# Performance work log

Measured on AMD Instinct MI355X. Metric: run time of the kernel, lower is better.

Reference implementation:

```python
import jax, jax.numpy as jnp
import numpy as np

B, T, D, NH = 4, 2048, 1024, 16
DH = D // NH


def setup_inputs() -> dict:
    key = jax.random.key(0)
    k1, k2, k3 = jax.random.split(key, 3)
    x = jax.random.normal(k1, (B, T, D), dtype=jnp.float32)
    # torch nn.Linear default init scale ~ 1/sqrt(fan_in); keep values sane
    w_qkv = jax.random.normal(k2, (D, 3 * D), dtype=jnp.float32) / np.sqrt(D)
    w_out = jax.random.normal(k3, (D, D), dtype=jnp.float32) / np.sqrt(D)
    return {"x": x, "w_qkv": w_qkv, "w_out": w_out}


def reference(x, w_qkv, w_out):
    Bb, Tt, Dd = x.shape
    # fused QKV projection (Linear, no bias)
    qkv = x @ w_qkv                                  # (B, T, 3D)
    q, k, v = jnp.split(qkv, 3, axis=-1)
    # split heads -> (B, NH, T, DH)
    q = q.reshape(Bb, Tt, NH, DH).transpose(0, 2, 1, 3)
    k = k.reshape(Bb, Tt, NH, DH).transpose(0, 2, 1, 3)
    v = v.reshape(Bb, Tt, NH, DH).transpose(0, 2, 1, 3)
    scale = 1.0 / np.sqrt(DH).astype(np.float32)
    att = jnp.einsum('bhqd,bhkd->bhqk', q, k) * scale  # (B, NH, T, T)
    att = jax.nn.softmax(att, axis=-1)
    y = jnp.einsum('bhqk,bhkd->bhqd', att, v)          # (B, NH, T, DH)
    y = y.transpose(0, 2, 1, 3).reshape(Bb, Tt, Dd)    # merge heads
    return y @ w_out                                   # output projection
```

## Files before the change

kernel.cpp:

```cpp
#include <hip/hip_runtime.h>

#define B  4
#define T  2048
#define D  1024
#define NH 16
#define DH 64
#define MROWS (B*T)

typedef __attribute__((ext_vector_type(8))) short bf16x8;
typedef __attribute__((ext_vector_type(4))) float f32x4;
typedef __attribute__((ext_vector_type(4))) unsigned short u16x4;
typedef __attribute__((address_space(1))) const void gvoid;
typedef __attribute__((address_space(3))) void lvoid;

#define C_EXP 0.18033688011112042f
#define VSWZ(dh) (((((dh) ^ ((dh) >> 2)) & 7)) << 4)

__device__ inline unsigned short f2bf(float f) {
    union { float f; unsigned int u; } v; v.f = f;
    unsigned int r = v.u + 0x7fff + ((v.u >> 16) & 1);
    return (unsigned short)(r >> 16);
}
__device__ inline float bf2f(unsigned short u) {
    union { unsigned int u; float f; } v; v.u = ((unsigned int)u) << 16;
    return v.f;
}
__device__ inline float exp2_fast(float x) {
    float r;
    asm("v_exp_f32 %0, %1" : "=v"(r) : "v"(x));
    return r;
}

__global__ __launch_bounds__(256)
void cast_bf16(const float* __restrict__ in, unsigned short* __restrict__ hi, int n4) {
    for (int i = blockIdx.x * 256 + threadIdx.x; i < n4; i += gridDim.x * 256) {
        const float4 v = ((const float4*)in)[i];
        ushort4 h;
        h.x = f2bf(v.x); h.y = f2bf(v.y); h.z = f2bf(v.z); h.w = f2bf(v.w);
        ((ushort4*)hi)[i] = h;
    }
}

__global__ __launch_bounds__(256)
void split_frag2(const float* __restrict__ Wq, const float* __restrict__ Wo,
                 unsigned short* __restrict__ fq, unsigned short* __restrict__ fo) {
    const int l   = threadIdx.x & 63;
    const int kt  = blockIdx.y;
    const int NKT = D / 32;
    const bool isQ = (blockIdx.x < 3 * D / 64);
    const int bx  = isQ ? blockIdx.x : blockIdx.x - 3 * D / 64;
    const int nt  = bx * 4 + (threadIdx.x >> 6);
    const int N   = isQ ? 3 * D : D;
    const float* Wm = isQ ? Wq : Wo;
    unsigned short* fh = isQ ? fq : fo;
    const int n   = nt * 16 + (l & 15);
    const int k0  = kt * 32 + (l >> 4) * 8;
    const float sc = (isQ && n < D) ? C_EXP : 1.0f;
    bf16x8 hv;
    #pragma unroll
    for (int j = 0; j < 8; ++j)
        hv[j] = (short)f2bf(Wm[(size_t)(k0 + j) * N + n] * sc);
    const size_t o = ((size_t)nt * NKT + kt) * 512 + (size_t)l * 8;
    *(bf16x8*)&fh[o] = hv;
}

template<bool OUT_BF16, bool TWO_PASS>
__global__ __launch_bounds__(256, 3)
void gemm_bdir(const unsigned short* __restrict__ Ahi, const unsigned short* __restrict__ Alo,
               const unsigned short* __restrict__ Bfh,
               void* __restrict__ Cout, int M, int N, int K) {
    __shared__ unsigned char As[2][128 * 128];
    const int tid  = threadIdx.x;
    const int w    = tid >> 6;
    const int lane = tid & 63;
    const int lq   = lane & 15;
    const int lk   = lane >> 4;
    const int wm   = w >> 1;
    const int wn   = w & 1;
    const int NKT  = K / 32;

    const int gx  = gridDim.x;
    const int cpx = gx >> 3;
    const int lin = blockIdx.y * gx + blockIdx.x;
    const int cx  = lin & 7;
    const int j   = lin >> 3;
    const int bn  = (cx * cpx + j % cpx) * 128;
    const int bm  = (j / cpx) * 128;

    const int srow   = lane >> 3;
    const int sidx   = (lane & 7) ^ srow;
    const int shalf  = sidx >> 2;
    const int schunk = sidx & 3;
    const unsigned short* aPtr = TWO_PASS
        ? ((shalf ? Alo : Ahi) + (size_t)(bm + w * 32 + srow) * K + schunk * 8)
        : (Ahi + (size_t)(bm + w * 32 + srow) * K + sidx * 8);

    const unsigned short* bhBase = Bfh + ((size_t)(bn / 16 + wn * 4) * NKT) * 512 + (size_t)lane * 8;

    f32x4 acc[4][4];
    #pragma unroll
    for (int m = 0; m < 4; ++m)
        #pragma unroll
        for (int n = 0; n < 4; ++n) acc[m][n] = f32x4{0.f, 0.f, 0.f, 0.f};

    #pragma unroll
    for (int i = 0; i < 4; ++i)
        __builtin_amdgcn_global_load_lds((gvoid*)(aPtr + (size_t)i * 8 * K),
                                         (lvoid*)&As[0][(w * 32 + i * 8) * 128], 16, 0, 0);
    __syncthreads();

    int cur = 0;
    if constexpr (TWO_PASS) {
        for (int kt = 0; kt < NKT; ++kt) {
            if (kt + 1 < NKT) {
                #pragma unroll
                for (int i = 0; i < 4; ++i)
                    __builtin_amdgcn_global_load_lds(
                        (gvoid*)(aPtr + (size_t)i * 8 * K + (kt + 1) * 32),
                        (lvoid*)&As[cur ^ 1][(w * 32 + i * 8) * 128], 16, 0, 0);
            }
            bf16x8 bh[4];
            #pragma unroll
            for (int n = 0; n < 4; ++n)
                bh[n] = *(const bf16x8*)&bhBase[((size_t)n * NKT + kt) * 512];
            bf16x8 ah[4], al[4];
            #pragma unroll
            for (int m = 0; m < 4; ++m) {
                const int row = wm * 64 + m * 16 + lq;
                const int sw  = row & 7;
                ah[m] = *(const bf16x8*)&As[cur][row * 128 + ((lk ^ sw) << 4)];
                al[m] = *(const bf16x8*)&As[cur][row * 128 + (((4 + lk) ^ sw) << 4)];
            }
            __builtin_amdgcn_s_setprio(1);
            #pragma unroll
            for (int n = 0; n < 4; ++n)
                #pragma unroll
                for (int m = 0; m < 4; ++m) {
                    acc[m][n] = __builtin_amdgcn_mfma_f32_16x16x32_bf16(ah[m], bh[n], acc[m][n], 0, 0, 0);
                    acc[m][n] = __builtin_amdgcn_mfma_f32_16x16x32_bf16(al[m], bh[n], acc[m][n], 0, 0, 0);
                }
            __builtin_amdgcn_s_setprio(0);
            __syncthreads();
            cur ^= 1;
        }
    } else {
        const int NS = K / 64;
        for (int s2 = 0; s2 < NS; ++s2) {
            if (s2 + 1 < NS) {
                #pragma unroll
                for (int i = 0; i < 4; ++i)
                    __builtin_amdgcn_global_load_lds(
                        (gvoid*)(aPtr + (size_t)i * 8 * K + (s2 + 1) * 64),
                        (lvoid*)&As[cur ^ 1][(w * 32 + i * 8) * 128], 16, 0, 0);
            }
            bf16x8 bh[4], bh2[4];
            #pragma unroll
            for (int n = 0; n < 4; ++n) {
                bh [n] = *(const bf16x8*)&bhBase[((size_t)n * NKT + 2 * s2    ) * 512];
                bh2[n] = *(const bf16x8*)&bhBase[((size_t)n * NKT + 2 * s2 + 1) * 512];
            }
            bf16x8 ah[4], al[4];
            #pragma unroll
            for (int m = 0; m < 4; ++m) {
                const int row = wm * 64 + m * 16 + lq;
                const int sw  = row & 7;
                ah[m] = *(const bf16x8*)&As[cur][row * 128 + ((lk ^ sw) << 4)];
                al[m] = *(const bf16x8*)&As[cur][row * 128 + (((4 + lk) ^ sw) << 4)];
            }
            __builtin_amdgcn_s_setprio(1);
            #pragma unroll
            for (int n = 0; n < 4; ++n)
                #pragma unroll
                for (int m = 0; m < 4; ++m) {
                    acc[m][n] = __builtin_amdgcn_mfma_f32_16x16x32_bf16(ah[m], bh [n], acc[m][n], 0, 0, 0);
                    acc[m][n] = __builtin_amdgcn_mfma_f32_16x16x32_bf16(al[m], bh2[n], acc[m][n], 0, 0, 0);
                }
            __builtin_amdgcn_s_setprio(0);
            __syncthreads();
            cur ^= 1;
        }
    }

    #pragma unroll
    for (int m = 0; m < 4; ++m)
        #pragma unroll
        for (int ri = 0; ri < 4; ++ri) {
            const int row = bm + wm * 64 + m * 16 + lk * 4 + ri;
            #pragma unroll
            for (int n = 0; n < 4; ++n) {
                const int col = bn + wn * 64 + n * 16 + lq;
                if (OUT_BF16)
                    ((unsigned short*)Cout)[(size_t)row * N + col] = f2bf(acc[m][n][ri]);
                else
                    ((float*)Cout)[(size_t)row * N + col] = acc[m][n][ri];
            }
        }
}

__global__ __launch_bounds__(512)
void attn_mfma(const unsigned short* __restrict__ qkv,
               unsigned short* __restrict__ yhi, unsigned short* __restrict__ ylo) {
    const int bh  = blockIdx.y;
    const int b   = bh / NH;
    const int h   = bh % NH;
    const int qt  = blockIdx.x;
    const int tid = threadIdx.x;
    const int w    = tid >> 6;
    const int lane = tid & 63;
    const int lq   = lane & 15;
    const int lk   = lane >> 4;

    __shared__ unsigned char Ks [64 * 128];
    __shared__ unsigned char Vts[2][64 * 128];
    __shared__ unsigned char Ps [8 * 2048];

    const unsigned short* qRow = qkv + (size_t)(b * T + qt * 128 + w * 16 + lq) * (3 * D) + h * DH + lk * 8;
    bf16x8 qf[2];
    qf[0] = *(const bf16x8*)(qRow);
    qf[1] = *(const bf16x8*)(qRow + 32);

    bf16x8 vones;
    #pragma unroll
    for (int j = 0; j < 8; ++j) vones[j] = (short)0x3F80;

    const int srow   = lane >> 3;
    const int schunk = (lane & 7) ^ srow;
    const unsigned short* kBase = qkv + (size_t)(b * T + w * 8 + srow) * (3 * D) + D + h * DH + schunk * 8;
    const unsigned short* vBase = qkv + (size_t)(b * T + w * 8 + lk * 2) * (3 * D) + 2 * D + h * DH + lq * 4;

    __builtin_amdgcn_global_load_lds((gvoid*)kBase, (lvoid*)&Ks[(w * 8) * 128], 16, 0, 0);
    u16x4 vr[2];
    #pragma unroll
    for (int i = 0; i < 2; ++i)
        vr[i] = *(const u16x4*)(vBase + (size_t)i * (3 * D));
    #pragma unroll
    for (int j = 0; j < 4; ++j) {
        const int dh = lq * 4 + j;
        const unsigned int pk = (unsigned int)vr[0][j] | ((unsigned int)vr[1][j] << 16);
        *(unsigned int*)&Vts[0][(dh * 128 + w * 16 + lk * 4) ^ VSWZ(dh)] = pk;
    }
    __syncthreads();

    f32x4 o[4];
    #pragma unroll
    for (int dt = 0; dt < 4; ++dt) o[dt] = f32x4{0.f, 0.f, 0.f, 0.f};
    f32x4 l_acc = f32x4{0.f, 0.f, 0.f, 0.f};

    unsigned char* Pw = &Ps[w * 2048];

    for (int t = 0; t < T / 64; ++t) {
        const int c = t & 1;
        const bool more = (t + 1 < T / 64);

        f32x4 s[4];
        #pragma unroll
        for (int ct = 0; ct < 4; ++ct) s[ct] = f32x4{0.f, 0.f, 0.f, 0.f};
        __builtin_amdgcn_s_setprio(1);
        #pragma unroll
        for (int ks = 0; ks < 2; ++ks) {
            #pragma unroll
            for (int ct = 0; ct < 4; ++ct) {
                const int key = ct * 16 + lq;
                const bf16x8 kf = *(const bf16x8*)&Ks[key * 128 + (((ks * 4 + lk) ^ (key & 7)) << 4)];
                s[ct] = __builtin_amdgcn_mfma_f32_16x16x32_bf16(kf, qf[ks], s[ct], 0, 0, 0);
            }
        }
        __builtin_amdgcn_s_setprio(0);
        __syncthreads();

        if (more) {
            const int ktn = (t + 1) * 64;
            __builtin_amdgcn_global_load_lds((gvoid*)(kBase + (size_t)ktn * (3 * D)),
                                             (lvoid*)&Ks[(w * 8) * 128], 16, 0, 0);
            #pragma unroll
            for (int i = 0; i < 2; ++i)
                vr[i] = *(const u16x4*)(vBase + (size_t)(ktn + i) * (3 * D));
        }

        float p[4][4];
        #pragma unroll
        for (int ct = 0; ct < 4; ++ct)
            #pragma unroll
            for (int r = 0; r < 4; ++r)
                p[ct][r] = exp2_fast(s[ct][r]);

        #pragma unroll
        for (int ct = 0; ct < 4; ++ct) {
            uint2 pk2;
            asm("v_cvt_pk_bf16_f32 %0, %1, %2" : "=v"(pk2.x) : "v"(p[ct][0]), "v"(p[ct][1]));
            asm("v_cvt_pk_bf16_f32 %0, %1, %2" : "=v"(pk2.y) : "v"(p[ct][2]), "v"(p[ct][3]));
            *(uint2*)&Pw[(lq * 128 + ct * 32 + lk * 8) ^ ((lq & 7) << 4)] = pk2;
        }
        asm volatile("s_waitcnt lgkmcnt(0)" ::: "memory");
        __builtin_amdgcn_sched_barrier(0);

        __builtin_amdgcn_s_setprio(1);
        #pragma unroll
        for (int ks = 0; ks < 2; ++ks) {
            const bf16x8 pf = *(const bf16x8*)&Pw[(lq * 128 + ks * 64 + lk * 16) ^ ((lq & 7) << 4)];
            #pragma unroll
            for (int dt = 0; dt < 4; ++dt) {
                const int dh = dt * 16 + lq;
                const bf16x8 vf = *(const bf16x8*)&Vts[c][(dh * 128 + ks * 64 + lk * 16) ^ VSWZ(dh)];
                o[dt] = __builtin_amdgcn_mfma_f32_16x16x32_bf16(pf, vf, o[dt], 0, 0, 0);
            }
            l_acc = __builtin_amdgcn_mfma_f32_16x16x32_bf16(pf, vones, l_acc, 0, 0, 0);
        }
        __builtin_amdgcn_s_setprio(0);

        if (more) {
            #pragma unroll
            for (int j = 0; j < 4; ++j) {
                const int dh = lq * 4 + j;
                const unsigned int pk = (unsigned int)vr[0][j] | ((unsigned int)vr[1][j] << 16);
                *(unsigned int*)&Vts[c ^ 1][(dh * 128 + w * 16 + lk * 4) ^ VSWZ(dh)] = pk;
            }
        }
        __syncthreads();
    }

    #pragma unroll
    for (int r = 0; r < 4; ++r) {
        const float inv = 1.0f / l_acc[r];
        const int row = qt * 128 + w * 16 + lk * 4 + r;
        const size_t base = (size_t)(b * T + row) * D + h * DH;
        #pragma unroll
        for (int dt = 0; dt < 4; ++dt) {
            const float val = o[dt][r] * inv;
            const unsigned short hv = f2bf(val);
            yhi[base + dt * 16 + lq] = hv;
            ylo[base + dt * 16 + lq] = f2bf(val - bf2f(hv));
        }
    }
}

extern "C" void kernel_launch(void* const* d_in, const int* in_sizes, int n_in,
                              void* d_out, int out_size, void* d_ws, size_t ws_size,
                              hipStream_t stream) {
    const float* x     = (const float*)d_in[0];
    const float* w_qkv = (const float*)d_in[1];
    const float* w_out = (const float*)d_in[2];

    unsigned short* Xhi = (unsigned short*)d_ws;
    unsigned short* Xlo = Xhi + (size_t)MROWS * D;
    unsigned short* Wqh = Xlo + (size_t)MROWS * D;
    unsigned short* Woh = Wqh + (size_t)3 * D * D;
    unsigned short* QKV = Woh + (size_t)D * D;

    cast_bf16<<<2048, 256, 0, stream>>>(x, Xhi, MROWS * D / 4);
    split_frag2<<<dim3(4 * D / 64, D / 32), 256, 0, stream>>>(w_qkv, w_out, Wqh, Woh);

    gemm_bdir<true, false><<<dim3(3 * D / 128, MROWS / 128), 256, 0, stream>>>(
        Xhi, Xlo, Wqh, QKV, MROWS, 3 * D, D);

    attn_mfma<<<dim3(T / 128, B * NH), 512, 0, stream>>>(QKV, Xhi, Xlo);

    gemm_bdir<false, true><<<dim3(D / 128, MROWS / 128), 256, 0, stream>>>(
        Xhi, Xlo, Woh, d_out, MROWS, D, D);
}
```

Measured before the change: 225.5 us.

## Halve attention block to 4 waves, each handling 32 query rows

Each wave now processes two 16-row query sub-tiles, so the block has 256 threads covering the same 128 queries. The K and V fragments read from LDS are reused across both sub-tiles, which halves LDS reads per MFMA, and launch bounds now ask for 3 blocks per CU. Each thread carries more accumulator registers, which raises register pressure and could limit occupancy. Fewer threads are also left to issue the K/V global loads.

```diff
diff --git a/kernel.cpp b/kernel.cpp
--- a/kernel.cpp
+++ b/kernel.cpp
@@ -197,7 +197,7 @@
         }
 }
 
-__global__ __launch_bounds__(512)
+__global__ __launch_bounds__(256, 3)
 void attn_mfma(const unsigned short* __restrict__ qkv,
                unsigned short* __restrict__ yhi, unsigned short* __restrict__ ylo) {
     const int bh  = blockIdx.y;
@@ -212,12 +212,16 @@
 
     __shared__ unsigned char Ks [64 * 128];
     __shared__ unsigned char Vts[2][64 * 128];
-    __shared__ unsigned char Ps [8 * 2048];
-
-    const unsigned short* qRow = qkv + (size_t)(b * T + qt * 128 + w * 16 + lq) * (3 * D) + h * DH + lk * 8;
-    bf16x8 qf[2];
-    qf[0] = *(const bf16x8*)(qRow);
-    qf[1] = *(const bf16x8*)(qRow + 32);
+    __shared__ unsigned char Ps [4 * 4096];
+
+    bf16x8 qf[2][2];
+    #pragma unroll
+    for (int qs = 0; qs < 2; ++qs) {
+        const unsigned short* qRow = qkv
+            + (size_t)(b * T + qt * 128 + w * 32 + qs * 16 + lq) * (3 * D) + h * DH + lk * 8;
+        qf[qs][0] = *(const bf16x8*)(qRow);
+        qf[qs][1] = *(const bf16x8*)(qRow + 32);
+    }
 
     bf16x8 vones;
     #pragma unroll
@@ -225,36 +229,47 @@
 
     const int srow   = lane >> 3;
     const int schunk = (lane & 7) ^ srow;
-    const unsigned short* kBase = qkv + (size_t)(b * T + w * 8 + srow) * (3 * D) + D + h * DH + schunk * 8;
-    const unsigned short* vBase = qkv + (size_t)(b * T + w * 8 + lk * 2) * (3 * D) + 2 * D + h * DH + lq * 4;
-
-    __builtin_amdgcn_global_load_lds((gvoid*)kBase, (lvoid*)&Ks[(w * 8) * 128], 16, 0, 0);
-    u16x4 vr[2];
+    const unsigned short* kBase = qkv + (size_t)(b * T + w * 16 + srow) * (3 * D) + D + h * DH + schunk * 8;
+    const unsigned short* vBase = qkv + (size_t)(b * T + w * 16 + lk * 4) * (3 * D) + 2 * D + h * DH + lq * 4;
+
     #pragma unroll
     for (int i = 0; i < 2; ++i)
+        __builtin_amdgcn_global_load_lds((gvoid*)(kBase + (size_t)i * 8 * (3 * D)),
+                                         (lvoid*)&Ks[(w * 16 + i * 8) * 128], 16, 0, 0);
+    u16x4 vr[4];
+    #pragma unroll
+    for (int i = 0; i < 4; ++i)
         vr[i] = *(const u16x4*)(vBase + (size_t)i * (3 * D));
     #pragma unroll
     for (int j = 0; j < 4; ++j) {
         const int dh = lq * 4 + j;
-        const unsigned int pk = (unsigned int)vr[0][j] | ((unsigned int)vr[1][j] << 16);
-        *(unsigned int*)&Vts[0][(dh * 128 + w * 16 + lk * 4) ^ VSWZ(dh)] = pk;
+        uint2 pk2;
+        pk2.x = (unsigned int)vr[0][j] | ((unsigned int)vr[1][j] << 16);
+        pk2.y = (unsigned int)vr[2][j] | ((unsigned int)vr[3][j] << 16);
+        *(uint2*)&Vts[0][(dh * 128 + w * 32 + lk * 8) ^ VSWZ(dh)] = pk2;
     }
     __syncthreads();
 
-    f32x4 o[4];
-    #pragma unroll
-    for (int dt = 0; dt < 4; ++dt) o[dt] = f32x4{0.f, 0.f, 0.f, 0.f};
-    f32x4 l_acc = f32x4{0.f, 0.f, 0.f, 0.f};
-
-    unsigned char* Pw = &Ps[w * 2048];
+    f32x4 o[2][4];
+    #pragma unroll
+    for (int qs = 0; qs < 2; ++qs)
+        #pragma unroll
+        for (int dt = 0; dt < 4; ++dt) o[qs][dt] = f32x4{0.f, 0.f, 0.f, 0.f};
+    f32x4 l_acc[2];
+    l_acc[0] = f32x4{0.f, 0.f, 0.f, 0.f};
+    l_acc[1] = f32x4{0.f, 0.f, 0.f, 0.f};
+
+    unsigned char* Pw = &Ps[w * 4096];
 
     for (int t = 0; t < T / 64; ++t) {
         const int c = t & 1;
         const bool more = (t + 1 < T / 64);
 
-        f32x4 s[4];
-        #pragma unroll
-        for (int ct = 0; ct < 4; ++ct) s[ct] = f32x4{0.f, 0.f, 0.f, 0.f};
+        f32x4 s[2][4];
+        #pragma unroll
+        for (int qs = 0; qs < 2; ++qs)
+            #pragma unroll
+            for (int ct = 0; ct < 4; ++ct) s[qs][ct] = f32x4{0.f, 0.f, 0.f, 0.f};
         __builtin_amdgcn_s_setprio(1);
         #pragma unroll
         for (int ks = 0; ks < 2; ++ks) {
@@ -262,7 +277,9 @@
             for (int ct = 0; ct < 4; ++ct) {
                 const int key = ct * 16 + lq;
                 const bf16x8 kf = *(const bf16x8*)&Ks[key * 128 + (((ks * 4 + lk) ^ (key & 7)) << 4)];
-                s[ct] = __builtin_amdgcn_mfma_f32_16x16x32_bf16(kf, qf[ks], s[ct], 0, 0, 0);
+                #pragma unroll
+                for (int qs = 0; qs < 2; ++qs)
+                    s[qs][ct] = __builtin_amdgcn_mfma_f32_16x16x32_bf16(kf, qf[qs][ks], s[qs][ct], 0, 0, 0);
             }
         }
         __builtin_amdgcn_s_setprio(0);
@@ -270,26 +287,35 @@
 
         if (more) {
             const int ktn = (t + 1) * 64;
-            __builtin_amdgcn_global_load_lds((gvoid*)(kBase + (size_t)ktn * (3 * D)),
-                                             (lvoid*)&Ks[(w * 8) * 128], 16, 0, 0);
             #pragma unroll
             for (int i = 0; i < 2; ++i)
+                __builtin_amdgcn_global_load_lds(
+                    (gvoid*)(kBase + (size_t)(ktn + i * 8) * (3 * D)),
+                    (lvoid*)&Ks[(w * 16 + i * 8) * 128], 16, 0, 0);
+            #pragma unroll
+            for (int i = 0; i < 4; ++i)
                 vr[i] = *(const u16x4*)(vBase + (size_t)(ktn + i) * (3 * D));
         }
 
-        float p[4][4];
-        #pragma unroll
-        for (int ct = 0; ct < 4; ++ct)
-            #pragma unroll
-            for (int r = 0; r < 4; ++r)
-                p[ct][r] = exp2_fast(s[ct][r]);
-
-        #pragma unroll
-        for (int ct = 0; ct < 4; ++ct) {
-            uint2 pk2;
-            asm("v_cvt_pk_bf16_f32 %0, %1, %2" : "=v"(pk2.x) : "v"(p[ct][0]), "v"(p[ct][1]));
-            asm("v_cvt_pk_bf16_f32 %0, %1, %2" : "=v"(pk2.y) : "v"(p[ct][2]), "v"(p[ct][3]));
-            *(uint2*)&Pw[(lq * 128 + ct * 32 + lk * 8) ^ ((lq & 7) << 4)] = pk2;
+        float p[2][4][4];
+        #pragma unroll
+        for (int qs = 0; qs < 2; ++qs)
+            #pragma unroll
+            for (int ct = 0; ct < 4; ++ct)
+                #pragma unroll
+                for (int r = 0; r < 4; ++r)
+                    p[qs][ct][r] = exp2_fast(s[qs][ct][r]);
+
+        #pragma unroll
+        for (int qs = 0; qs < 2; ++qs) {
+            const int row = qs * 16 + lq;
+            #pragma unroll
+            for (int ct = 0; ct < 4; ++ct) {
+                uint2 pk2;
+                asm("v_cvt_pk_bf16_f32 %0, %1, %2" : "=v"(pk2.x) : "v"(p[qs][ct][0]), "v"(p[qs][ct][1]));
+                asm("v_cvt_pk_bf16_f32 %0, %1, %2" : "=v"(pk2.y) : "v"(p[qs][ct][2]), "v"(p[qs][ct][3]));
+                *(uint2*)&Pw[(row * 128 + ct * 32 + lk * 8) ^ ((lq & 7) << 4)] = pk2;
+            }
         }
         asm volatile("s_waitcnt lgkmcnt(0)" ::: "memory");
         __builtin_amdgcn_sched_barrier(0);
@@ -297,14 +323,21 @@
         __builtin_amdgcn_s_setprio(1);
         #pragma unroll
         for (int ks = 0; ks < 2; ++ks) {
-            const bf16x8 pf = *(const bf16x8*)&Pw[(lq * 128 + ks * 64 + lk * 16) ^ ((lq & 7) << 4)];
+            bf16x8 vf[4];
             #pragma unroll
             for (int dt = 0; dt < 4; ++dt) {
                 const int dh = dt * 16 + lq;
-                const bf16x8 vf = *(const bf16x8*)&Vts[c][(dh * 128 + ks * 64 + lk * 16) ^ VSWZ(dh)];
-                o[dt] = __builtin_amdgcn_mfma_f32_16x16x32_bf16(pf, vf, o[dt], 0, 0, 0);
-            }
-            l_acc = __builtin_amdgcn_mfma_f32_16x16x32_bf16(pf, vones, l_acc, 0, 0, 0);
+                vf[dt] = *(const bf16x8*)&Vts[c][(dh * 128 + ks * 64 + lk * 16) ^ VSWZ(dh)];
+            }
+            #pragma unroll
+            for (int qs = 0; qs < 2; ++qs) {
+                const int row = qs * 16 + lq;
+                const bf16x8 pf = *(const bf16x8*)&Pw[(row * 128 + ks * 64 + lk * 16) ^ ((lq & 7) << 4)];
+                #pragma unroll
+                for (int dt = 0; dt < 4; ++dt)
+                    o[qs][dt] = __builtin_amdgcn_mfma_f32_16x16x32_bf16(pf, vf[dt], o[qs][dt], 0, 0, 0);
+                l_acc[qs] = __builtin_amdgcn_mfma_f32_16x16x32_bf16(pf, vones, l_acc[qs], 0, 0, 0);
+            }
         }
         __builtin_amdgcn_s_setprio(0);
 
@@ -312,26 +345,30 @@
             #pragma unroll
             for (int j = 0; j < 4; ++j) {
                 const int dh = lq * 4 + j;
-                const unsigned int pk = (unsigned int)vr[0][j] | ((unsigned int)vr[1][j] << 16);
-                *(unsigned int*)&Vts[c ^ 1][(dh * 128 + w * 16 + lk * 4) ^ VSWZ(dh)] = pk;
+                uint2 pk2;
+                pk2.x = (unsigned int)vr[0][j] | ((unsigned int)vr[1][j] << 16);
+                pk2.y = (unsigned int)vr[2][j] | ((unsigned int)vr[3][j] << 16);
+                *(uint2*)&Vts[c ^ 1][(dh * 128 + w * 32 + lk * 8) ^ VSWZ(dh)] = pk2;
             }
         }
         __syncthreads();
     }
 
     #pragma unroll
-    for (int r = 0; r < 4; ++r) {
-        const float inv = 1.0f / l_acc[r];
-        const int row = qt * 128 + w * 16 + lk * 4 + r;
-        const size_t base = (size_t)(b * T + row) * D + h * DH;
-        #pragma unroll
-        for (int dt = 0; dt < 4; ++dt) {
-            const float val = o[dt][r] * inv;
-            const unsigned short hv = f2bf(val);
-            yhi[base + dt * 16 + lq] = hv;
-            ylo[base + dt * 16 + lq] = f2bf(val - bf2f(hv));
-        }
-    }
+    for (int qs = 0; qs < 2; ++qs)
+        #pragma unroll
+        for (int r = 0; r < 4; ++r) {
+            const float inv = 1.0f / l_acc[qs][r];
+            const int row = qt * 128 + w * 32 + qs * 16 + lk * 4 + r;
+            const size_t base = (size_t)(b * T + row) * D + h * DH;
+            #pragma unroll
+            for (int dt = 0; dt < 4; ++dt) {
+                const float val = o[qs][dt][r] * inv;
+                const unsigned short hv = f2bf(val);
+                yhi[base + dt * 16 + lq] = hv;
+                ylo[base + dt * 16 + lq] = f2bf(val - bf2f(hv));
+            }
+        }
 }
 
 extern "C" void kernel_launch(void* const* d_in, const int* in_sizes, int n_in,
@@ -353,7 +390,7 @@
     gemm_bdir<true, false><<<dim3(3 * D / 128, MROWS / 128), 256, 0, stream>>>(
         Xhi, Xlo, Wqh, QKV, MROWS, 3 * D, D);
 
-    attn_mfma<<<dim3(T / 128, B * NH), 512, 0, stream>>>(QKV, Xhi, Xlo);
+    attn_mfma<<<dim3(T / 128, B * NH), 256, 0, stream>>>(QKV, Xhi, Xlo);
 
     gemm_bdir<false, true><<<dim3(D / 128, MROWS / 128), 256, 0, stream>>>(
         Xhi, Xlo, Woh, d_out, MROWS, D, D);
```

Measured after the change: 220.0 us. 1.02x faster.
